# Kernel optimization log

Hardware: AMD Instinct MI355X
Metric: run time of the kernel (lower is better)

## Reference

```python
import jax, jax.numpy as jnp
import numpy as np
from jax import lax

S, T, B = 32, 32, 512          # src len, tgt len, batch
H, E, A = 1024, 256, 1024      # hidden, embed, attention dim
VS, VT = 64, 70                # source / target char vocab
START = 1                      # data.tar_l2i[start_token]


def _gru_cell(gi, h, W_hh, b_hh):
    """torch GRUCell math. gi = x @ W_ih.T + b_ih, shape (B, 3H)."""
    gh = h @ W_hh.T + b_hh
    ir, iz, in_ = jnp.split(gi, 3, axis=-1)
    hr, hz, hn = jnp.split(gh, 3, axis=-1)
    r = jax.nn.sigmoid(ir + hr)
    z = jax.nn.sigmoid(iz + hz)
    n = jnp.tanh(in_ + r * hn)
    return (1.0 - z) * n + z * h


def setup_inputs() -> dict:
    key = jax.random.key(0)
    ks = jax.random.split(key, 16)
    n = lambda k, shp: jax.random.normal(k, shp, dtype=jnp.float32) * 0.05
    return {
        "source": jax.random.randint(ks[0], (S, B), 0, VS),
        "target": jax.random.randint(ks[1], (T, B), 0, VT),
        "teacher_forcing": 1,
        "emb_src": n(ks[2], (VS, E)),
        "W_ih_enc": n(ks[3], (3 * H, E)),
        "W_hh_enc": n(ks[4], (3 * H, H)),
        "b_ih_enc": n(ks[5], (3 * H,)),
        "b_hh_enc": n(ks[6], (3 * H,)),
        "emb_tgt": n(ks[7], (VT, E)),
        "W_attn": n(ks[8], (2 * H, A)),
        "b_attn": n(ks[9], (A,)),
        "v_attn": n(ks[10], (A,)),
        "W_ih_dec": n(ks[11], (3 * H, H + E)),
        "W_hh_dec": n(ks[12], (3 * H, H)),
        "b_ih_dec": n(ks[13], (3 * H,)),
        "b_hh_dec": n(ks[14], (3 * H,)),
        "W_out": n(ks[15], (H, VT)),
        "b_out": jnp.zeros((VT,), jnp.float32),
    }


def reference(source, target, teacher_forcing, emb_src, W_ih_enc, W_hh_enc,
              b_ih_enc, b_hh_enc, emb_tgt, W_attn, b_attn, v_attn,
              W_ih_dec, W_hh_dec, b_ih_dec, b_hh_dec, W_out, b_out):
    tf = bool(teacher_forcing)

    # ---------------- Encoder: GRU over (S, B) ----------------
    x_emb = emb_src[source]                                   # (S, B, E)
    # precompute input-to-hidden GEMM for all timesteps (big fused GEMM)
    gi_all = jnp.einsum('sbe,ge->sbg', x_emb, W_ih_enc) + b_ih_enc  # (S, B, 3H)

    def enc_step(h, gi_t):
        h = _gru_cell(gi_t, h, W_hh_enc, b_hh_enc)
        return h, h

    h0 = jnp.zeros((B, H), x_emb.dtype)
    h_enc, enc_ops = lax.scan(enc_step, h0, gi_all)           # enc_ops: (S, B, H)

    # ---------------- Decoder loop (t = 1 .. T-1) ----------------
    def dec_step(carry, tgt_t):
        h, x = carry
        emb = emb_tgt[x]                                      # (B, E)
        hx = jnp.broadcast_to(h[None], (S, B, H))
        feat = jnp.concatenate([hx, enc_ops], axis=-1)        # (S, B, 2H)
        energy = jnp.tanh(jnp.einsum('sbf,fa->sba', feat, W_attn) + b_attn)
        scores = energy @ v_attn                              # (S, B)
        alpha = jax.nn.softmax(scores, axis=0)                # over source positions
        ctx = jnp.einsum('sb,sbh->bh', alpha, enc_ops)        # (B, H)
        gi = jnp.concatenate([ctx, emb], axis=-1) @ W_ih_dec.T + b_ih_dec
        h_new = _gru_cell(gi, h, W_hh_dec, b_hh_dec)
        logits = h_new @ W_out + b_out                        # (B, VT)
        x_next = tgt_t if tf else jnp.argmax(logits, axis=1)
        return (h_new, x_next), (logits, alpha.T)             # attn row: (B, S)

    (_, _), (dec_logits, attn) = lax.scan(dec_step, (h_enc, target[0]), target[1:])

    # outputs[0] is the one-hot start token (outputs[:, :, start]=1, rows 1.. overwritten)
    row0 = jnp.zeros((B, VT), dec_logits.dtype).at[:, START].set(1.0)
    outputs = jnp.concatenate([row0[None], dec_logits], axis=0)  # (T, B, VT)
    return outputs, attn                                         # attn: (T-1, B, S)
```

## Files before the change

kernel.cpp:

```cpp
#include <hip/hip_runtime.h>
#include <hip/hip_bf16.h>

typedef __bf16 bfx8 __attribute__((ext_vector_type(8)));
typedef __bf16 bfx4 __attribute__((ext_vector_type(4)));
typedef float f32x4 __attribute__((ext_vector_type(4)));

#define MFMA __builtin_amdgcn_mfma_f32_16x16x32_bf16


__device__ __attribute__((aligned(256))) float  g_h[512 * 1024];
__device__ __attribute__((aligned(256))) float  g_hpart[512 * 1024];
__device__ __attribute__((aligned(256))) __bf16 g_hb[2][512 * 1024];
__device__ __attribute__((aligned(256))) __bf16 g_Adec[512 * 1280];
__device__ __attribute__((aligned(256))) __bf16 g_enc_ops[(size_t)32 * 512 * 1024];
__device__ __attribute__((aligned(256))) __bf16 g_enc_part[(size_t)32 * 512 * 1024];
__device__ __attribute__((aligned(256))) __bf16 g_WattnT[(size_t)1024 * 2048];
__device__ __attribute__((aligned(256))) __bf16 g_sWhhe[(size_t)3072 * 1024];
__device__ __attribute__((aligned(256))) __bf16 g_sWihe[(size_t)3072 * 256];
__device__ __attribute__((aligned(256))) __bf16 g_sWhhd[(size_t)3072 * 1024];
__device__ __attribute__((aligned(256))) __bf16 g_sWihd[(size_t)3072 * 1280];
__device__ __attribute__((aligned(256))) __bf16 g_sWattnA[(size_t)1024 * 1024];
__device__ __attribute__((aligned(256))) __bf16 g_sWout[(size_t)128 * 1024];
__device__ __attribute__((aligned(256))) __bf16 g_embs[64 * 256];
__device__ __attribute__((aligned(256))) __bf16 g_embt[70 * 256];

__device__ __forceinline__ float fast_tanh(float x) {
    float cx = fminf(fmaxf(x, -15.f), 15.f);
    float e = __expf(-2.f * cx);
    return (1.f - e) / (1.f + e);
}

__global__ void k_cvt(const float* __restrict__ src, __bf16* __restrict__ dst,
                      int n4)
{
    int i = blockIdx.x * 256 + threadIdx.x;
    if (i >= n4) return;
    float4 v = ((const float4*)src)[i];
    __bf16 o[4] = {(__bf16)v.x, (__bf16)v.y, (__bf16)v.z, (__bf16)v.w};
    *(ushort2*)(dst + 4 * i) = *(ushort2*)o;
    *(ushort2*)(dst + 4 * i + 2) = *(ushort2*)(o + 2);
}

__global__ void swz_rm(const float* __restrict__ W, __bf16* __restrict__ out,
                       int nK, int total)
{
    int gid = blockIdx.x * 256 + threadIdx.x;
    if (gid >= total) return;
    int F = gid >> 6, L = gid & 63;
    int t = F / nK, c = F - t * nK;
    int K = nK * 32;
    const float* s = W + (size_t)(t * 16 + (L & 15)) * K + c * 32 + (L >> 4) * 8;
    __bf16 o[8];
#pragma unroll
    for (int u = 0; u < 8; u++) o[u] = (__bf16)s[u];
    *(uint4*)(out + (size_t)gid * 8) = *(uint4*)o;
}

__global__ void swz_cm(const float* __restrict__ W, __bf16* __restrict__ out,
                       int nK, int ldsrc, int nguard, int total)
{
    int gid = blockIdx.x * 256 + threadIdx.x;
    if (gid >= total) return;
    int F = gid >> 6, L = gid & 63;
    int t = F / nK, c = F - t * nK;
    int n = t * 16 + (L & 15);
    int k = c * 32 + (L >> 4) * 8;
    __bf16 o[8];
#pragma unroll
    for (int u = 0; u < 8; u++)
        o[u] = (n < nguard) ? (__bf16)W[(size_t)(k + u) * ldsrc + n] : (__bf16)0.f;
    *(uint4*)(out + (size_t)gid * 8) = *(uint4*)o;
}

__global__ __launch_bounds__(256) void k_transpose(const float* __restrict__ Wsrc)
{
    __shared__ float t[32][33];
    int bx = blockIdx.x, by = blockIdx.y;
    int lx = threadIdx.x & 31, ly = threadIdx.x >> 5;
    for (int i = 0; i < 32; i += 8)
        t[ly + i][lx] = Wsrc[(size_t)(by * 32 + ly + i) * 1024 + bx * 32 + lx];
    __syncthreads();
    for (int i = 0; i < 32; i += 8)
        g_WattnT[(size_t)(bx * 32 + ly + i) * 2048 + by * 32 + lx] =
            (__bf16)t[lx][ly + i];
}

__global__ void k_init(float* __restrict__ out)
{
    int idx = blockIdx.x * 256 + threadIdx.x;
    if (idx < 512 * 1024) { g_h[idx] = 0.f; g_hb[0][idx] = (__bf16)0.f; }
    if (idx < 512 * 70) out[idx] = (idx % 70 == 1) ? 1.f : 0.f;
}

__global__ __launch_bounds__(256) void gemm_bt(
    const __bf16* __restrict__ Amat, int lda,
    const __bf16* __restrict__ Wmat, int ldw,
    const float* __restrict__ bias,
    void* __restrict__ Cout, int ldc, int cmode, int K, int nguard)
{
    __shared__ __bf16 As[64][40];
    __shared__ __bf16 Ws[64][40];
    const int tid  = threadIdx.x;
    const int m0   = blockIdx.y * 64;
    const int n0   = blockIdx.x * 64;
    const int wave = tid >> 6;
    const int lane = tid & 63;
    const int srow = tid >> 2;
    const int scol = (tid & 3) << 3;

    const __bf16* aptr = Amat + (size_t)(m0 + srow) * lda + scol;
    const __bf16* wptr = Wmat + (size_t)(n0 + srow) * ldw + scol;

    f32x4 acc[4];
#pragma unroll
    for (int i = 0; i < 4; i++) acc[i] = (f32x4){0.f, 0.f, 0.f, 0.f};

    const int r15 = lane & 15;
    const int kk  = (lane >> 4) << 3;

    for (int k0 = 0; k0 < K; k0 += 32) {
        uint4 av = *(const uint4*)(aptr + k0);
        uint4 wv = *(const uint4*)(wptr + k0);
        __syncthreads();
        *(uint4*)(&As[srow][scol]) = av;
        *(uint4*)(&Ws[srow][scol]) = wv;
        __syncthreads();
        bfx8 a = *(const bfx8*)(&As[wave * 16 + r15][kk]);
#pragma unroll
        for (int n = 0; n < 4; n++) {
            bfx8 b = *(const bfx8*)(&Ws[n * 16 + r15][kk]);
            acc[n] = MFMA(a, b, acc[n], 0, 0, 0);
        }
    }

    const int rowb = m0 + wave * 16 + (lane >> 4) * 4;
#pragma unroll
    for (int n = 0; n < 4; n++) {
        int c = n0 + n * 16 + r15;
        if (c >= nguard) continue;
        float bv = bias ? bias[c] : 0.f;
#pragma unroll
        for (int r = 0; r < 4; r++) {
            float v = acc[n][r] + bv;
            size_t off = (size_t)(rowb + r) * ldc + c;
            if (cmode == 0) ((float*)Cout)[off] = v;
            else            ((__bf16*)Cout)[off] = (__bf16)v;
        }
    }
}

__global__ __launch_bounds__(512, 1) void gru_step(
    const __bf16* __restrict__ hb_in, __bf16* __restrict__ hb_out,
    const __bf16* __restrict__ sW1, const float* __restrict__ b1,
    const __bf16* __restrict__ sW2, const float* __restrict__ b2,
    int nK2, const int* __restrict__ src_t, int enc_t)
{
    __shared__ __bf16 sA1[32 * 1024];
    __shared__ __bf16 sA2[32 * 1280];
    const int tid = threadIdx.x;
    const int w = tid >> 6, lane = tid & 63;
    const int r15 = lane & 15, q = lane >> 4;
    const int j0 = blockIdx.x * 64, m0 = blockIdx.y * 32;
    const int jsub = w & 3;

#pragma unroll
    for (int i = 0; i < 8; i++) {
        int lin = tid + i * 512;
        int r = lin >> 7, U = lin & 127;
        uint4 v = *(const uint4*)(hb_in + (size_t)(m0 + r) * 1024 + U * 8);
        *(uint4*)(sA1 + (r * 128 + (U ^ (r & 7))) * 8) = v;
    }
    if (src_t) {
#pragma unroll
        for (int i = 0; i < 2; i++) {
            int lin = tid + i * 512;
            int r = lin >> 5, U = lin & 31;
            int sv = src_t[m0 + r];
            sv = (sv < 0) ? 0 : (sv > 63 ? 63 : sv);
            uint4 v = *(const uint4*)(g_embs + sv * 256 + U * 8);
            *(uint4*)(sA2 + (r * 32 + (U ^ (r & 7))) * 8) = v;
        }
    } else {
        for (int lin = tid; lin < 32 * 160; lin += 512) {
            int r = lin / 160, U = lin - r * 160;
            uint4 v = *(const uint4*)(g_Adec + (size_t)(m0 + r) * 1280 + U * 8);
            *(uint4*)(sA2 + (r * 160 + (U ^ (r & 7))) * 8) = v;
        }
    }
    __syncthreads();

    const size_t tb = (size_t)(blockIdx.x * 4 + jsub);
    const int xk = r15 & 7;
    f32x4 acc[3][2];
#pragma unroll
    for (int s = 0; s < 3; s++)
#pragma unroll
        for (int ms = 0; ms < 2; ms++) acc[s][ms] = (f32x4){0.f, 0.f, 0.f, 0.f};

    if (w < 4) {
        const __bf16* wp0 = sW1 + (tb * 32) * 512 + lane * 8;
        const __bf16* wp1 = sW1 + ((tb + 64) * 32) * 512 + lane * 8;
        const __bf16* wp2 = sW1 + ((tb + 128) * 32) * 512 + lane * 8;
        const int ar0 = r15 * 1024, ar1 = (16 + r15) * 1024;
#pragma unroll 4
        for (int c = 0; c < 32; c++) {
            int us = ((c * 4 + q) ^ xk) * 8;
            bfx8 a0 = *(const bfx8*)(sA1 + ar0 + us);
            bfx8 a1 = *(const bfx8*)(sA1 + ar1 + us);
            bfx8 w0 = *(const bfx8*)(wp0 + c * 512);
            bfx8 w1 = *(const bfx8*)(wp1 + c * 512);
            bfx8 w2 = *(const bfx8*)(wp2 + c * 512);
            acc[0][0] = MFMA(a0, w0, acc[0][0], 0, 0, 0);
            acc[0][1] = MFMA(a1, w0, acc[0][1], 0, 0, 0);
            acc[1][0] = MFMA(a0, w1, acc[1][0], 0, 0, 0);
            acc[1][1] = MFMA(a1, w1, acc[1][1], 0, 0, 0);
            acc[2][0] = MFMA(a0, w2, acc[2][0], 0, 0, 0);
            acc[2][1] = MFMA(a1, w2, acc[2][1], 0, 0, 0);
        }
    } else {
        const __bf16* wp0 = sW2 + (tb * (size_t)nK2) * 512 + lane * 8;
        const __bf16* wp1 = sW2 + ((tb + 64) * (size_t)nK2) * 512 + lane * 8;
        const __bf16* wp2 = sW2 + ((tb + 128) * (size_t)nK2) * 512 + lane * 8;
        const int ru = nK2 * 4;
        const int ar0 = r15 * ru * 8, ar1 = (16 + r15) * ru * 8;
#pragma unroll 4
        for (int c = 0; c < nK2; c++) {
            int us = ((c * 4 + q) ^ xk) * 8;
            bfx8 a0 = *(const bfx8*)(sA2 + ar0 + us);
            bfx8 a1 = *(const bfx8*)(sA2 + ar1 + us);
            bfx8 w0 = *(const bfx8*)(wp0 + c * 512);
            bfx8 w1 = *(const bfx8*)(wp1 + c * 512);
            bfx8 w2 = *(const bfx8*)(wp2 + c * 512);
            acc[0][0] = MFMA(a0, w0, acc[0][0], 0, 0, 0);
            acc[0][1] = MFMA(a1, w0, acc[0][1], 0, 0, 0);
            acc[1][0] = MFMA(a0, w1, acc[1][0], 0, 0, 0);
            acc[1][1] = MFMA(a1, w1, acc[1][1], 0, 0, 0);
            acc[2][0] = MFMA(a0, w2, acc[2][0], 0, 0, 0);
            acc[2][1] = MFMA(a1, w2, acc[2][1], 0, 0, 0);
        }
    }
    __syncthreads();
    float* sGi = (float*)sA2;
    if (w >= 4) {
#pragma unroll
        for (int s = 0; s < 3; s++)
#pragma unroll
            for (int ms = 0; ms < 2; ms++)
#pragma unroll
                for (int reg = 0; reg < 4; reg++)
                    sGi[((s * 4 + jsub) * 32 + ms * 16 + q * 4 + reg) * 16 + r15] =
                        acc[s][ms][reg];
    }
    __syncthreads();
    if (w < 4) {
        const int jj = j0 + jsub * 16 + r15;
        const float bb1[3] = {b1[jj], b1[1024 + jj], b1[2048 + jj]};
        const float bb2[3] = {b2[jj], b2[1024 + jj], b2[2048 + jj]};
#pragma unroll
        for (int ms = 0; ms < 2; ms++) {
#pragma unroll
            for (int reg = 0; reg < 4; reg++) {
                int bl = ms * 16 + q * 4 + reg;
                int b_ = m0 + bl;
                float gh0 = acc[0][ms][reg] + bb1[0];
                float gh1 = acc[1][ms][reg] + bb1[1];
                float gh2 = acc[2][ms][reg] + bb1[2];
                float gi0 = sGi[((0 * 4 + jsub) * 32 + bl) * 16 + r15] + bb2[0];
                float gi1 = sGi[((1 * 4 + jsub) * 32 + bl) * 16 + r15] + bb2[1];
                float gi2 = sGi[((2 * 4 + jsub) * 32 + bl) * 16 + r15] + bb2[2];
                float r = 1.f / (1.f + __expf(-(gi0 + gh0)));
                float z = 1.f / (1.f + __expf(-(gi1 + gh1)));
                float n = fast_tanh(gi2 + r * gh2);
                size_t off = (size_t)b_ * 1024 + jj;
                float hv = (1.f - z) * n + z * g_h[off];
                g_h[off] = hv;
                hb_out[off] = (__bf16)hv;
                if (enc_t >= 0)
                    g_enc_ops[(size_t)enc_t * 524288 + off] = (__bf16)hv;
            }
        }
    }
}

__global__ __launch_bounds__(256) void k_hl(
    const __bf16* __restrict__ src, const float* __restrict__ battn,
    const float* __restrict__ bout, int lrow, float* __restrict__ outp)
{
    __shared__ __bf16 sA[32 * 1024];
    const int tid = threadIdx.x;
    const int w = tid >> 6, lane = tid & 63;
    const int r15 = lane & 15, q = lane >> 4;
    const int bx = blockIdx.x, m0 = blockIdx.y * 32;

#pragma unroll
    for (int i = 0; i < 16; i++) {
        int lin = tid + i * 256;
        int r = lin >> 7, U = lin & 127;
        uint4 v = *(const uint4*)(src + (size_t)(m0 + r) * 1024 + U * 8);
        *(uint4*)(sA + (r * 128 + (U ^ (r & 7))) * 8) = v;
    }
    __syncthreads();

    const __bf16* sW;
    int n;
    if (bx < 16) {
        sW = g_sWattnA;
        n = bx * 64 + w * 16 + r15;
    } else {
        if (lrow < 0) return;
        sW = g_sWout;
        n = (bx - 16) * 64 + w * 16 + r15;
    }
    const size_t tb = (size_t)((bx < 16 ? bx : bx - 16) * 4 + w);
    const __bf16* wp = sW + (tb * 32) * 512 + lane * 8;
    const int xk = r15 & 7;
    const int ar0 = r15 * 1024, ar1 = (16 + r15) * 1024;

    f32x4 acc[2];
    acc[0] = (f32x4){0.f, 0.f, 0.f, 0.f};
    acc[1] = (f32x4){0.f, 0.f, 0.f, 0.f};
#pragma unroll 4
    for (int c = 0; c < 32; c++) {
        int us = ((c * 4 + q) ^ xk) * 8;
        bfx8 a0 = *(const bfx8*)(sA + ar0 + us);
        bfx8 a1 = *(const bfx8*)(sA + ar1 + us);
        bfx8 wv = *(const bfx8*)(wp + c * 512);
        acc[0] = MFMA(a0, wv, acc[0], 0, 0, 0);
        acc[1] = MFMA(a1, wv, acc[1], 0, 0, 0);
    }

    if (bx < 16) {
        float bv = battn[n];
#pragma unroll
        for (int ms = 0; ms < 2; ms++)
#pragma unroll
            for (int reg = 0; reg < 4; reg++)
                g_hpart[(size_t)(m0 + ms * 16 + q * 4 + reg) * 1024 + n] =
                    acc[ms][reg] + bv;
    } else if (n < 70) {
        float bv = bout[n];
#pragma unroll
        for (int ms = 0; ms < 2; ms++)
#pragma unroll
            for (int reg = 0; reg < 4; reg++)
                outp[(size_t)lrow * 35840 +
                     (size_t)(m0 + ms * 16 + q * 4 + reg) * 70 + n] =
                    acc[ms][reg] + bv;
    }
}

__global__ __launch_bounds__(256) void k_attn(
    int j, const int* __restrict__ target, const int* __restrict__ tf,
    const float* __restrict__ v_attn, float* __restrict__ out)
{
    const int b = blockIdx.x, tid = threadIdx.x;
    const int lane = tid & 63, wave = tid >> 6;
    __shared__ float sc[32], sal[32];
    __shared__ int sx;
    if (wave == 0) {
        int xv;
        if (j == 0) xv = target[b];
        else if (*tf) xv = target[j * 512 + b];
        else {
            const float* row = out + (size_t)j * 35840 + b * 70;
            float bv = row[lane]; int bi = lane;
            if (lane < 6) {
                float v2 = row[lane + 64];
                if (v2 > bv) { bv = v2; bi = lane + 64; }
            }
#pragma unroll
            for (int off = 32; off; off >>= 1) {
                float ov = __shfl_down(bv, off);
                int   oi = __shfl_down(bi, off);
                if (ov > bv || (ov == bv && oi < bi)) { bv = ov; bi = oi; }
            }
            xv = bi;
        }
        if (lane == 0) sx = (xv < 0) ? 0 : (xv > 69 ? 69 : xv);
    }
    float hpv[16], vsv[16];
    {
        const float* hp = g_hpart + (size_t)b * 1024;
#pragma unroll
        for (int u = 0; u < 8; u++) {
            hpv[u]     = hp[lane * 8 + u];
            hpv[8 + u] = hp[512 + lane * 8 + u];
            vsv[u]     = v_attn[lane * 8 + u];
            vsv[8 + u] = v_attn[512 + lane * 8 + u];
        }
    }
    __syncthreads();
    g_Adec[(size_t)b * 1280 + 1024 + tid] = g_embt[sx * 256 + tid];
    for (int s = wave * 8; s < wave * 8 + 8; s++) {
        const __bf16* ep = g_enc_part + ((size_t)s * 512 + b) * 1024;
        bfx8 e0 = *(const bfx8*)(ep + lane * 8);
        bfx8 e1 = *(const bfx8*)(ep + 512 + lane * 8);
        float part = 0.f;
#pragma unroll
        for (int u = 0; u < 8; u++) {
            part += vsv[u]     * fast_tanh((float)e0[u] + hpv[u]);
            part += vsv[8 + u] * fast_tanh((float)e1[u] + hpv[8 + u]);
        }
#pragma unroll
        for (int off = 32; off; off >>= 1) part += __shfl_down(part, off);
        if (lane == 0) sc[s] = part;
    }
    __syncthreads();
    float mx = sc[0];
#pragma unroll
    for (int s = 1; s < 32; s++) mx = fmaxf(mx, sc[s]);
    float den = 0.f;
#pragma unroll
    for (int s = 0; s < 32; s++) den += __expf(sc[s] - mx);
    float rden = 1.f / den;
    if (tid < 32) {
        float al = __expf(sc[tid] - mx) * rden;
        sal[tid] = al;
        out[1146880 + (size_t)j * 16384 + b * 32 + tid] = al;
    }
    __syncthreads();
    float c0 = 0, c1 = 0, c2 = 0, c3 = 0;
    const __bf16* eo = g_enc_ops + (size_t)b * 1024 + tid * 4;
#pragma unroll 4
    for (int s = 0; s < 32; s++) {
        bfx4 e = *(const bfx4*)(eo + (size_t)s * 524288);
        float al = sal[s];
        c0 += al * (float)e[0]; c1 += al * (float)e[1];
        c2 += al * (float)e[2]; c3 += al * (float)e[3];
    }
    bfx4 o = {(__bf16)c0, (__bf16)c1, (__bf16)c2, (__bf16)c3};
    *(bfx4*)(&g_Adec[(size_t)b * 1280 + tid * 4]) = o;
}

extern "C" void kernel_launch(void* const* d_in, const int* in_sizes, int n_in,
                              void* d_out, int out_size, void* d_ws, size_t ws_size,
                              hipStream_t stream)
{
    const int*   source   = (const int*)d_in[0];
    const int*   target   = (const int*)d_in[1];
    const int*   tf       = (const int*)d_in[2];
    const float* emb_src  = (const float*)d_in[3];
    const float* W_ih_enc = (const float*)d_in[4];
    const float* W_hh_enc = (const float*)d_in[5];
    const float* b_ih_enc = (const float*)d_in[6];
    const float* b_hh_enc = (const float*)d_in[7];
    const float* emb_tgt  = (const float*)d_in[8];
    const float* W_attn   = (const float*)d_in[9];
    const float* b_attn   = (const float*)d_in[10];
    const float* v_attn   = (const float*)d_in[11];
    const float* W_ih_dec = (const float*)d_in[12];
    const float* W_hh_dec = (const float*)d_in[13];
    const float* b_ih_dec = (const float*)d_in[14];
    const float* b_hh_dec = (const float*)d_in[15];
    const float* W_out    = (const float*)d_in[16];
    const float* b_out    = (const float*)d_in[17];
    float* out = (float*)d_out;

    void *p_hb, *p_sWhhe, *p_sWihe, *p_sWhhd, *p_sWihd, *p_sWattnA, *p_sWout,
         *p_embs, *p_embt, *p_WattnT, *p_enc_ops, *p_enc_part;
    hipGetSymbolAddress(&p_hb,       HIP_SYMBOL(g_hb));
    hipGetSymbolAddress(&p_sWhhe,    HIP_SYMBOL(g_sWhhe));
    hipGetSymbolAddress(&p_sWihe,    HIP_SYMBOL(g_sWihe));
    hipGetSymbolAddress(&p_sWhhd,    HIP_SYMBOL(g_sWhhd));
    hipGetSymbolAddress(&p_sWihd,    HIP_SYMBOL(g_sWihd));
    hipGetSymbolAddress(&p_sWattnA,  HIP_SYMBOL(g_sWattnA));
    hipGetSymbolAddress(&p_sWout,    HIP_SYMBOL(g_sWout));
    hipGetSymbolAddress(&p_embs,     HIP_SYMBOL(g_embs));
    hipGetSymbolAddress(&p_embt,     HIP_SYMBOL(g_embt));
    hipGetSymbolAddress(&p_WattnT,   HIP_SYMBOL(g_WattnT));
    hipGetSymbolAddress(&p_enc_ops,  HIP_SYMBOL(g_enc_ops));
    hipGetSymbolAddress(&p_enc_part, HIP_SYMBOL(g_enc_part));
    __bf16* hb0 = (__bf16*)p_hb;
    __bf16* hb1 = hb0 + 512 * 1024;

    k_cvt<<<16, 256, 0, stream>>>(emb_src, (__bf16*)p_embs, 64 * 256 / 4);
    k_cvt<<<18, 256, 0, stream>>>(emb_tgt, (__bf16*)p_embt, 70 * 256 / 4);
    swz_rm<<<1536, 256, 0, stream>>>(W_hh_enc, (__bf16*)p_sWhhe, 32, 393216);
    swz_rm<<<384,  256, 0, stream>>>(W_ih_enc, (__bf16*)p_sWihe, 8,  98304);
    swz_rm<<<1536, 256, 0, stream>>>(W_hh_dec, (__bf16*)p_sWhhd, 32, 393216);
    swz_rm<<<1920, 256, 0, stream>>>(W_ih_dec, (__bf16*)p_sWihd, 40, 491520);
    swz_cm<<<512,  256, 0, stream>>>(W_attn, (__bf16*)p_sWattnA, 32, 1024, 1024, 131072);
    swz_cm<<<64,   256, 0, stream>>>(W_out,  (__bf16*)p_sWout,   32, 70,   70,   16384);
    k_transpose<<<dim3(32, 64), 256, 0, stream>>>(W_attn);
    k_init<<<2048, 256, 0, stream>>>(out);

    for (int t = 0; t < 32; t++) {
        __bf16* hin  = (t & 1) ? hb1 : hb0;
        __bf16* hout = (t & 1) ? hb0 : hb1;
        gru_step<<<dim3(16, 16), 512, 0, stream>>>(
            hin, hout, (__bf16*)p_sWhhe, b_hh_enc,
            (__bf16*)p_sWihe, b_ih_enc, 8, source + t * 512, t);
    }

    gemm_bt<<<dim3(16, 256), 256, 0, stream>>>(
        (__bf16*)p_enc_ops, 1024, (__bf16*)p_WattnT + 1024, 2048, nullptr,
        p_enc_part, 1024, 1, 1024, 1 << 30);

    k_hl<<<dim3(18, 16), 256, 0, stream>>>(hb0, b_attn, b_out, -1, out);

    for (int j = 0; j < 31; j++) {
        __bf16* hin  = (j & 1) ? hb1 : hb0;
        __bf16* hout = (j & 1) ? hb0 : hb1;
        k_attn<<<512, 256, 0, stream>>>(j, target, tf, v_attn, out);
        gru_step<<<dim3(16, 16), 512, 0, stream>>>(
            hin, hout, (__bf16*)p_sWhhd, b_hh_dec,
            (__bf16*)p_sWihd, b_ih_dec, 40, nullptr, -1);
        k_hl<<<dim3(18, 16), 256, 0, stream>>>(hout, b_attn, b_out, j + 1, out);
    }
}
```

Before: 2.521 ms.

## Replace encoder-part attention GEMM with swizzled-weight, LDS-resident A tile kernel

```diff
diff --git a/kernel.cpp b/kernel.cpp
--- a/kernel.cpp
+++ b/kernel.cpp
@@ -14,12 +14,12 @@
 __device__ __attribute__((aligned(256))) __bf16 g_Adec[512 * 1280];
 __device__ __attribute__((aligned(256))) __bf16 g_enc_ops[(size_t)32 * 512 * 1024];
 __device__ __attribute__((aligned(256))) __bf16 g_enc_part[(size_t)32 * 512 * 1024];
-__device__ __attribute__((aligned(256))) __bf16 g_WattnT[(size_t)1024 * 2048];
 __device__ __attribute__((aligned(256))) __bf16 g_sWhhe[(size_t)3072 * 1024];
 __device__ __attribute__((aligned(256))) __bf16 g_sWihe[(size_t)3072 * 256];
 __device__ __attribute__((aligned(256))) __bf16 g_sWhhd[(size_t)3072 * 1024];
 __device__ __attribute__((aligned(256))) __bf16 g_sWihd[(size_t)3072 * 1280];
 __device__ __attribute__((aligned(256))) __bf16 g_sWattnA[(size_t)1024 * 1024];
+__device__ __attribute__((aligned(256))) __bf16 g_sWattnB[(size_t)1024 * 1024];
 __device__ __attribute__((aligned(256))) __bf16 g_sWout[(size_t)128 * 1024];
 __device__ __attribute__((aligned(256))) __bf16 g_embs[64 * 256];
 __device__ __attribute__((aligned(256))) __bf16 g_embt[70 * 256];
@@ -72,19 +72,6 @@
     *(uint4*)(out + (size_t)gid * 8) = *(uint4*)o;
 }
 
-__global__ __launch_bounds__(256) void k_transpose(const float* __restrict__ Wsrc)
-{
-    __shared__ float t[32][33];
-    int bx = blockIdx.x, by = blockIdx.y;
-    int lx = threadIdx.x & 31, ly = threadIdx.x >> 5;
-    for (int i = 0; i < 32; i += 8)
-        t[ly + i][lx] = Wsrc[(size_t)(by * 32 + ly + i) * 1024 + bx * 32 + lx];
-    __syncthreads();
-    for (int i = 0; i < 32; i += 8)
-        g_WattnT[(size_t)(bx * 32 + ly + i) * 2048 + by * 32 + lx] =
-            (__bf16)t[lx][ly + i];
-}
-
 __global__ void k_init(float* __restrict__ out)
 {
     int idx = blockIdx.x * 256 + threadIdx.x;
@@ -92,59 +79,68 @@
     if (idx < 512 * 70) out[idx] = (idx % 70 == 1) ? 1.f : 0.f;
 }
 
-__global__ __launch_bounds__(256) void gemm_bt(
-    const __bf16* __restrict__ Amat, int lda,
-    const __bf16* __restrict__ Wmat, int ldw,
-    const float* __restrict__ bias,
-    void* __restrict__ Cout, int ldc, int cmode, int K, int nguard)
-{
-    __shared__ __bf16 As[64][40];
-    __shared__ __bf16 Ws[64][40];
-    const int tid  = threadIdx.x;
-    const int m0   = blockIdx.y * 64;
-    const int n0   = blockIdx.x * 64;
-    const int wave = tid >> 6;
-    const int lane = tid & 63;
-    const int srow = tid >> 2;
-    const int scol = (tid & 3) << 3;
-
-    const __bf16* aptr = Amat + (size_t)(m0 + srow) * lda + scol;
-    const __bf16* wptr = Wmat + (size_t)(n0 + srow) * ldw + scol;
-
-    f32x4 acc[4];
-#pragma unroll
-    for (int i = 0; i < 4; i++) acc[i] = (f32x4){0.f, 0.f, 0.f, 0.f};
-
-    const int r15 = lane & 15;
-    const int kk  = (lane >> 4) << 3;
-
-    for (int k0 = 0; k0 < K; k0 += 32) {
-        uint4 av = *(const uint4*)(aptr + k0);
-        uint4 wv = *(const uint4*)(wptr + k0);
-        __syncthreads();
-        *(uint4*)(&As[srow][scol]) = av;
-        *(uint4*)(&Ws[srow][scol]) = wv;
-        __syncthreads();
-        bfx8 a = *(const bfx8*)(&As[wave * 16 + r15][kk]);
-#pragma unroll
-        for (int n = 0; n < 4; n++) {
-            bfx8 b = *(const bfx8*)(&Ws[n * 16 + r15][kk]);
-            acc[n] = MFMA(a, b, acc[n], 0, 0, 0);
-        }
-    }
-
-    const int rowb = m0 + wave * 16 + (lane >> 4) * 4;
-#pragma unroll
-    for (int n = 0; n < 4; n++) {
-        int c = n0 + n * 16 + r15;
-        if (c >= nguard) continue;
-        float bv = bias ? bias[c] : 0.f;
-#pragma unroll
-        for (int r = 0; r < 4; r++) {
-            float v = acc[n][r] + bv;
-            size_t off = (size_t)(rowb + r) * ldc + c;
-            if (cmode == 0) ((float*)Cout)[off] = v;
-            else            ((__bf16*)Cout)[off] = (__bf16)v;
+__global__ __launch_bounds__(512, 1) void k_encpart(
+    const __bf16* __restrict__ Amat, const __bf16* __restrict__ sW,
+    __bf16* __restrict__ Cout)
+{
+    __shared__ __bf16 sA[64 * 1024];
+    const int tid = threadIdx.x;
+    const int w = tid >> 6, lane = tid & 63;
+    const int r15 = lane & 15, q = lane >> 4;
+    const int n0 = blockIdx.x * 256, m0 = blockIdx.y * 64;
+
+#pragma unroll
+    for (int i = 0; i < 16; i++) {
+        int lin = tid + i * 512;
+        int r = lin >> 7, U = lin & 127;
+        uint4 v = *(const uint4*)(Amat + (size_t)(m0 + r) * 1024 + U * 8);
+        *(uint4*)(sA + (r * 128 + (U ^ (r & 7))) * 8) = v;
+    }
+    __syncthreads();
+
+    const int xk = r15 & 7;
+    f32x4 acc[2][4];
+#pragma unroll
+    for (int nn = 0; nn < 2; nn++)
+#pragma unroll
+        for (int mf = 0; mf < 4; mf++) acc[nn][mf] = (f32x4){0.f, 0.f, 0.f, 0.f};
+
+    const __bf16* wp0 = sW + ((size_t)(blockIdx.x * 16 + w * 2) * 32) * 512 + lane * 8;
+    const __bf16* wp1 = wp0 + 32 * 512;
+    const int ar0 = r15 * 1024;
+    const int ar1 = (16 + r15) * 1024;
+    const int ar2 = (32 + r15) * 1024;
+    const int ar3 = (48 + r15) * 1024;
+
+#pragma unroll 4
+    for (int c = 0; c < 32; c++) {
+        int us = ((c * 4 + q) ^ xk) * 8;
+        bfx8 a0 = *(const bfx8*)(sA + ar0 + us);
+        bfx8 a1 = *(const bfx8*)(sA + ar1 + us);
+        bfx8 a2 = *(const bfx8*)(sA + ar2 + us);
+        bfx8 a3 = *(const bfx8*)(sA + ar3 + us);
+        bfx8 w0 = *(const bfx8*)(wp0 + c * 512);
+        bfx8 w1 = *(const bfx8*)(wp1 + c * 512);
+        acc[0][0] = MFMA(a0, w0, acc[0][0], 0, 0, 0);
+        acc[0][1] = MFMA(a1, w0, acc[0][1], 0, 0, 0);
+        acc[0][2] = MFMA(a2, w0, acc[0][2], 0, 0, 0);
+        acc[0][3] = MFMA(a3, w0, acc[0][3], 0, 0, 0);
+        acc[1][0] = MFMA(a0, w1, acc[1][0], 0, 0, 0);
+        acc[1][1] = MFMA(a1, w1, acc[1][1], 0, 0, 0);
+        acc[1][2] = MFMA(a2, w1, acc[1][2], 0, 0, 0);
+        acc[1][3] = MFMA(a3, w1, acc[1][3], 0, 0, 0);
+    }
+
+#pragma unroll
+    for (int nn = 0; nn < 2; nn++) {
+        const int col = n0 + (w * 2 + nn) * 16 + r15;
+#pragma unroll
+        for (int mf = 0; mf < 4; mf++) {
+#pragma unroll
+            for (int reg = 0; reg < 4; reg++) {
+                int row = m0 + mf * 16 + q * 4 + reg;
+                Cout[(size_t)row * 1024 + col] = (__bf16)acc[nn][mf][reg];
+            }
         }
     }
 }
@@ -456,18 +452,18 @@
     const float* b_out    = (const float*)d_in[17];
     float* out = (float*)d_out;
 
-    void *p_hb, *p_sWhhe, *p_sWihe, *p_sWhhd, *p_sWihd, *p_sWattnA, *p_sWout,
-         *p_embs, *p_embt, *p_WattnT, *p_enc_ops, *p_enc_part;
+    void *p_hb, *p_sWhhe, *p_sWihe, *p_sWhhd, *p_sWihd, *p_sWattnA, *p_sWattnB,
+         *p_sWout, *p_embs, *p_embt, *p_enc_ops, *p_enc_part;
     hipGetSymbolAddress(&p_hb,       HIP_SYMBOL(g_hb));
     hipGetSymbolAddress(&p_sWhhe,    HIP_SYMBOL(g_sWhhe));
     hipGetSymbolAddress(&p_sWihe,    HIP_SYMBOL(g_sWihe));
     hipGetSymbolAddress(&p_sWhhd,    HIP_SYMBOL(g_sWhhd));
     hipGetSymbolAddress(&p_sWihd,    HIP_SYMBOL(g_sWihd));
     hipGetSymbolAddress(&p_sWattnA,  HIP_SYMBOL(g_sWattnA));
+    hipGetSymbolAddress(&p_sWattnB,  HIP_SYMBOL(g_sWattnB));
     hipGetSymbolAddress(&p_sWout,    HIP_SYMBOL(g_sWout));
     hipGetSymbolAddress(&p_embs,     HIP_SYMBOL(g_embs));
     hipGetSymbolAddress(&p_embt,     HIP_SYMBOL(g_embt));
-    hipGetSymbolAddress(&p_WattnT,   HIP_SYMBOL(g_WattnT));
     hipGetSymbolAddress(&p_enc_ops,  HIP_SYMBOL(g_enc_ops));
     hipGetSymbolAddress(&p_enc_part, HIP_SYMBOL(g_enc_part));
     __bf16* hb0 = (__bf16*)p_hb;
@@ -480,8 +476,9 @@
     swz_rm<<<1536, 256, 0, stream>>>(W_hh_dec, (__bf16*)p_sWhhd, 32, 393216);
     swz_rm<<<1920, 256, 0, stream>>>(W_ih_dec, (__bf16*)p_sWihd, 40, 491520);
     swz_cm<<<512,  256, 0, stream>>>(W_attn, (__bf16*)p_sWattnA, 32, 1024, 1024, 131072);
+    swz_cm<<<512,  256, 0, stream>>>(W_attn + (size_t)1024 * 1024,
+                                     (__bf16*)p_sWattnB, 32, 1024, 1024, 131072);
     swz_cm<<<64,   256, 0, stream>>>(W_out,  (__bf16*)p_sWout,   32, 70,   70,   16384);
-    k_transpose<<<dim3(32, 64), 256, 0, stream>>>(W_attn);
     k_init<<<2048, 256, 0, stream>>>(out);
 
     for (int t = 0; t < 32; t++) {
@@ -492,9 +489,8 @@
             (__bf16*)p_sWihe, b_ih_enc, 8, source + t * 512, t);
     }
 
-    gemm_bt<<<dim3(16, 256), 256, 0, stream>>>(
-        (__bf16*)p_enc_ops, 1024, (__bf16*)p_WattnT + 1024, 2048, nullptr,
-        p_enc_part, 1024, 1, 1024, 1 << 30);
+    k_encpart<<<dim3(4, 256), 512, 0, stream>>>(
+        (__bf16*)p_enc_ops, (__bf16*)p_sWattnB, (__bf16*)p_enc_part);
 
     k_hl<<<dim3(18, 16), 256, 0, stream>>>(hb0, b_attn, b_out, -1, out);
 
```

Result: no change. 2.551 ms (+1.2%).
